# Performance work log

Measured on AMD Instinct MI355X. Metric: run time of the kernel, lower is better.

## Reference

```python
import jax, jax.numpy as jnp
import numpy as np

H = 256          # hidden_size
K = 3            # pointer hops
LAMDA = 3.0
EPS = 1e-8       # torch cosine_similarity eps
# dropout is treated as eval-mode (identity)


def _gru_cell(x, h, wi, wh, bi, bh):
    # torch GRUCell: gate order reset, update, new
    gx = x @ wi.T + bi            # (B, 3*4H)
    gh = h @ wh.T + bh
    xr, xz, xn = jnp.split(gx, 3, axis=-1)
    hr, hz, hn = jnp.split(gh, 3, axis=-1)
    r = jax.nn.sigmoid(xr + hr)
    z = jax.nn.sigmoid(xz + hz)
    n = jnp.tanh(xn + r * hn)
    return (1.0 - z) * n + z * h


def setup_inputs() -> dict:
    key = jax.random.key(0)
    ks = jax.random.split(key, 16)
    B, L = 128, 512
    d2, d4 = 2 * H, 4 * H
    sc = lambda i, shape, fan: jax.random.normal(ks[i], shape, jnp.float32) * (1.0 / np.sqrt(fan))
    return {
        "m": jax.random.normal(ks[0], (B, L, d2), jnp.float32),
        "s1": jax.random.normal(ks[1], (B, d4), jnp.float32),
        "s2": jax.random.normal(ks[2], (B, d4), jnp.float32),
        "s3": jax.random.normal(ks[3], (B, d4), jnp.float32),
        "m_mask": jnp.ones((B, L), jnp.int32),
        "w2_w": sc(4, (d2, d2), d2), "w2_b": jnp.zeros((d2,), jnp.float32),
        "w3_w": sc(5, (d4, d2), d4), "w3_b": jnp.zeros((d2,), jnp.float32),
        "w4_w": sc(6, (d4, d4), d4), "w4_b": jnp.zeros((d4,), jnp.float32),
        "w5_w": sc(7, (d4, 1), d4), "w5_b": jnp.zeros((1,), jnp.float32),
        "gru_wi": sc(8, (3 * d4, d2), d2),
        "gru_wh": sc(9, (3 * d4, d4), d4),
        "gru_bi": jnp.zeros((3 * d4,), jnp.float32),
        "gru_bh": jnp.zeros((3 * d4,), jnp.float32),
    }


def reference(m, s1, s2, s3, m_mask,
              w2_w, w2_b, w3_w, w3_b, w4_w, w4_b, w5_w, w5_b,
              gru_wi, gru_wh, gru_bi, gru_bh):
    # m: (B, L, 2H); s*: (B, 4H); m_mask: (B, L)
    mtt = m @ w2_w + w2_b                         # (B, L, 2H), loop-invariant
    m_norm = jnp.maximum(jnp.linalg.norm(mtt, axis=-1), EPS)  # (B, L)
    invalid = m_mask == 0

    def branch(st):
        for _ in range(K):
            stt = st @ w3_w + w3_b                # (B, 2H)
            s_norm = jnp.maximum(jnp.linalg.norm(stt, axis=-1), EPS)  # (B,)
            dot = jnp.einsum('bld,bd->bl', mtt, stt)
            att = LAMDA * dot / (m_norm * s_norm[:, None])
            att = jnp.where(invalid, -jnp.inf, att)
            p = jax.nn.softmax(att, axis=1)       # (B, L)
            f_att = jnp.einsum('bl,bld->bd', p, m)  # (B, 2H)
            st = _gru_cell(f_att, st, gru_wi, gru_wh, gru_bi, gru_bh)
        h = jax.nn.relu(st @ w4_w + w4_b)         # (B, 4H)
        return (h @ w5_w + w5_b)[:, 0]            # (B,)

    result = jnp.stack([branch(s1), branch(s2), branch(s3)], axis=1)  # (B, 3)
    return jax.nn.log_softmax(result, axis=1)
```

## Files before the change

kernel.cpp:

```cpp
#include <hip/hip_runtime.h>
#include <math.h>

constexpr int B  = 128;
constexpr int L  = 512;
constexpr int D2 = 512;
constexpr int D4 = 1024;
constexpr int G3 = 3072;
constexpr int R3 = 384;
constexpr int NC = 4096;
constexpr float LAMDA = 3.0f;
constexpr float EPSF  = 1e-8f;

typedef __attribute__((ext_vector_type(8))) short bf16x8;
typedef __attribute__((ext_vector_type(8))) short short8;
typedef __attribute__((ext_vector_type(4))) float f32x4;

__device__ __forceinline__ ushort f2bf(float v) {
  uint u = __builtin_bit_cast(uint, v);
  u = (u + 0x7fffu + ((u >> 16) & 1u)) >> 16;
  return (ushort)u;
}
__device__ __forceinline__ float bf2f(ushort h) {
  return __builtin_bit_cast(float, (uint)h << 16);
}
__device__ __forceinline__ float bflo(uint w) { return __builtin_bit_cast(float, w << 16); }
__device__ __forceinline__ float bfhi(uint w) { return __builtin_bit_cast(float, w & 0xffff0000u); }
__device__ __forceinline__ void split2(float v, ushort& h, ushort& l) {
  h = f2bf(v);
  l = f2bf(v - bf2f(h));
}
__device__ __forceinline__ void gload_lds16(const void* g, void* l) {
  __builtin_amdgcn_global_load_lds(
      (const __attribute__((address_space(1))) unsigned int*)g,
      (__attribute__((address_space(3))) unsigned int*)l, 16, 0, 0);
}

__global__ void k_init(const float* __restrict__ s1, const float* __restrict__ s2,
                       const float* __restrict__ s3, float* __restrict__ st3,
                       ushort* __restrict__ sth, ushort* __restrict__ stl,
                       float* __restrict__ snacc, float* __restrict__ cacc,
                       float* __restrict__ o3) {
  int idx = blockIdx.x * blockDim.x + threadIdx.x;
  if (idx < R3) { snacc[idx] = 0.f; cacc[idx] = 0.f; o3[idx] = 0.f; }
  int total = R3 * D4;
  for (; idx < total; idx += gridDim.x * blockDim.x) {
    int r = idx / D4, i = idx - r * D4;
    int k = r / B, b = r - k * B;
    const float* s = (k == 0) ? s1 : (k == 1) ? s2 : s3;
    float v = s[b * D4 + i];
    st3[idx] = v;
    if (sth) { ushort h, l; split2(v, h, l); sth[idx] = h; stl[idx] = l; }
  }
}

__global__ void k_conv_m(const float* __restrict__ m, ushort* __restrict__ mbf) {
  int idx = blockIdx.x * blockDim.x + threadIdx.x;
  const int total8 = (B * L * D2) / 8;
  for (; idx < total8; idx += gridDim.x * blockDim.x) {
    const float4* p = reinterpret_cast<const float4*>(m) + (size_t)idx * 2;
    float4 a = p[0], c = p[1];
    ushort o[8] = {f2bf(a.x), f2bf(a.y), f2bf(a.z), f2bf(a.w),
                   f2bf(c.x), f2bf(c.y), f2bf(c.z), f2bf(c.w)};
    *reinterpret_cast<uint4*>(mbf + (size_t)idx * 8) = *reinterpret_cast<const uint4*>(o);
  }
}

__global__ void k_w2t(const float* __restrict__ w2, ushort* __restrict__ w2t) {
  __shared__ ushort t[64][65];
  int bk = (blockIdx.x & 7) * 64, bn = (blockIdx.x >> 3) * 64;
  int tid = threadIdx.x;
#pragma unroll
  for (int i = 0; i < 16; ++i) {
    int e = tid + i * 256; int r = e >> 6, c = e & 63;
    t[r][c] = f2bf(w2[(bk + r) * 512 + bn + c]);
  }
  __syncthreads();
#pragma unroll
  for (int i = 0; i < 16; ++i) {
    int e = tid + i * 256; int r = e >> 6, c = e & 63;
    w2t[(bn + r) * 512 + bk + c] = t[c][r];
  }
}

__global__ void k_split_direct(const float* __restrict__ in, ushort* __restrict__ oh,
                               ushort* __restrict__ ol, int n4) {
  int idx = blockIdx.x * blockDim.x + threadIdx.x;
  for (; idx < n4; idx += gridDim.x * blockDim.x) {
    float4 v = reinterpret_cast<const float4*>(in)[idx];
    ushort4 h, l;
    split2(v.x, h.x, l.x); split2(v.y, h.y, l.y);
    split2(v.z, h.z, l.z); split2(v.w, h.w, l.w);
    reinterpret_cast<ushort4*>(oh)[idx] = h;
    reinterpret_cast<ushort4*>(ol)[idx] = l;
  }
}

__global__ void k_split_trans(const float* __restrict__ in, int K, int N,
                              ushort* __restrict__ oh, ushort* __restrict__ ol) {
  __shared__ float t[64][65];
  int bk = blockIdx.x * 64, bn = blockIdx.y * 64;
  int tid = threadIdx.x;
#pragma unroll
  for (int i = 0; i < 16; ++i) {
    int e = tid + i * 256; int r = e >> 6, c = e & 63;
    t[r][c] = in[(size_t)(bk + r) * N + bn + c];
  }
  __syncthreads();
#pragma unroll
  for (int i = 0; i < 16; ++i) {
    int e = tid + i * 256; int r = e >> 6, c = e & 63;
    ushort h, l;
    split2(t[c][r], h, l);
    oh[(size_t)(bn + r) * K + bk + c] = h;
    ol[(size_t)(bn + r) * K + bk + c] = l;
  }
}

__global__ void k_bcat2(const float* __restrict__ w3b, const float* __restrict__ gbh,
                        const float* __restrict__ w2w, float* __restrict__ bcat) {
  int idx = blockIdx.x * 256 + threadIdx.x;
  if (idx < D2) bcat[idx] = w3b[idx];
  else if (idx < D2 + G3) bcat[idx] = gbh[idx - D2];
  else if (idx < NC) {
    int e = idx - (D2 + G3);
    float s = 0.f;
    for (int d = 0; d < D2; ++d) s = fmaf(w3b[d], w2w[(size_t)e * D2 + d], s);
    bcat[idx] = s;
  }
}

__global__ __launch_bounds__(64) void k_gemm_wf(
    const ushort* __restrict__ Ahp, const ushort* __restrict__ Alp,
    const ushort* __restrict__ Bhp, const ushort* __restrict__ Blp,
    ushort* __restrict__ Ch, ushort* __restrict__ Cl) {
  const int ln = threadIdx.x;
  const int lrow = ln & 15, lk = ln >> 4;
  const int rowb = blockIdx.y * 64;
  const int colb = blockIdx.x * 64;
  size_t aoff[4], boff[4];
#pragma unroll
  for (int f = 0; f < 4; ++f) {
    aoff[f] = (size_t)(rowb + f * 16 + lrow) * D2 + lk * 8;
    boff[f] = (size_t)(colb + f * 16 + lrow) * D2 + lk * 8;
  }
  f32x4 acc[4][4] = {};
  for (int kc = 0; kc < D2; kc += 32) {
    bf16x8 ah[4], al[4], bh[4], bl[4];
#pragma unroll
    for (int f = 0; f < 4; ++f) {
      ah[f] = *reinterpret_cast<const bf16x8*>(Ahp + aoff[f] + kc);
      al[f] = *reinterpret_cast<const bf16x8*>(Alp + aoff[f] + kc);
      bh[f] = *reinterpret_cast<const bf16x8*>(Bhp + boff[f] + kc);
      bl[f] = *reinterpret_cast<const bf16x8*>(Blp + boff[f] + kc);
    }
#pragma unroll
    for (int rf = 0; rf < 4; ++rf)
#pragma unroll
      for (int cf = 0; cf < 4; ++cf) {
        acc[rf][cf] = __builtin_amdgcn_mfma_f32_16x16x32_bf16(ah[rf], bh[cf], acc[rf][cf], 0, 0, 0);
        acc[rf][cf] = __builtin_amdgcn_mfma_f32_16x16x32_bf16(al[rf], bh[cf], acc[rf][cf], 0, 0, 0);
        acc[rf][cf] = __builtin_amdgcn_mfma_f32_16x16x32_bf16(ah[rf], bl[cf], acc[rf][cf], 0, 0, 0);
      }
  }
#pragma unroll
  for (int rf = 0; rf < 4; ++rf)
#pragma unroll
    for (int cf = 0; cf < 4; ++cf) {
      int col = colb + cf * 16 + lrow;
#pragma unroll
      for (int j = 0; j < 4; ++j) {
        int row = rowb + rf * 16 + lk * 4 + j;
        ushort h, l;
        split2(acc[rf][cf][j], h, l);
        Ch[(size_t)row * D4 + col] = h;
        Cl[(size_t)row * D4 + col] = l;
      }
    }
}

__global__ __launch_bounds__(256, 2) void k_mnorm4(const ushort* __restrict__ mbf,
                                                   const ushort* __restrict__ w2t,
                                                   const float* __restrict__ b2,
                                                   float* __restrict__ norm2) {
  __shared__ ushort As[2][64 * 32];
  __shared__ ushort Bs[2][512 * 32];
  const int tid = threadIdx.x;
  const int wv = tid >> 6, ln = tid & 63;
  const int lrow = ln & 15, lk = ln >> 4;
  const size_t rowb = (size_t)blockIdx.x * 64;

  auto stage = [&](int buf, int kc) {
    {
      int li = wv * 64 + ln;
      int row = li >> 2, slot = li & 3;
      const ushort* src = mbf + (rowb + row) * 512 + kc + ((slot ^ (row & 3)) << 3);
      gload_lds16(src, &As[buf][(size_t)wv * 64 * 8]);
    }
#pragma unroll
    for (int i = 0; i < 8; ++i) {
      int c = wv * 8 + i;
      int li = c * 64 + ln;
      int col = li >> 2, slot = li & 3;
      const ushort* src = w2t + (size_t)col * 512 + kc + ((slot ^ (col & 3)) << 3);
      gload_lds16(src, &Bs[buf][(size_t)c * 64 * 8]);
    }
  };

  f32x4 acc[4][8] = {};
  stage(0, 0);
  __syncthreads();
  for (int t = 0; t < 16; ++t) {
    int cur = t & 1;
    if (t + 1 < 16) stage(cur ^ 1, (t + 1) * 32);
    bf16x8 af[4], bfr[8];
#pragma unroll
    for (int rf = 0; rf < 4; ++rf) {
      int row = rf * 16 + lrow;
      af[rf] = *reinterpret_cast<const bf16x8*>(&As[cur][row * 32 + ((lk ^ (row & 3)) << 3)]);
    }
#pragma unroll
    for (int cf = 0; cf < 8; ++cf) {
      int col = wv * 128 + cf * 16 + lrow;
      bfr[cf] = *reinterpret_cast<const bf16x8*>(&Bs[cur][col * 32 + ((lk ^ (col & 3)) << 3)]);
    }
#pragma unroll
    for (int rf = 0; rf < 4; ++rf)
#pragma unroll
      for (int cf = 0; cf < 8; ++cf)
        acc[rf][cf] = __builtin_amdgcn_mfma_f32_16x16x32_bf16(af[rf], bfr[cf], acc[rf][cf], 0, 0, 0);
    __syncthreads();
  }

  float nrm[4][4] = {};
#pragma unroll
  for (int cf = 0; cf < 8; ++cf) {
    float bb = b2[wv * 128 + cf * 16 + lrow];
#pragma unroll
    for (int rf = 0; rf < 4; ++rf)
#pragma unroll
      for (int j = 0; j < 4; ++j) {
        float v = acc[rf][cf][j] + bb;
        nrm[rf][j] = fmaf(v, v, nrm[rf][j]);
      }
  }
  __shared__ float red[4][64];
#pragma unroll
  for (int rf = 0; rf < 4; ++rf)
#pragma unroll
    for (int j = 0; j < 4; ++j) {
      float v = nrm[rf][j];
      v += __shfl_xor(v, 1); v += __shfl_xor(v, 2);
      v += __shfl_xor(v, 4); v += __shfl_xor(v, 8);
      if (lrow == 0) red[wv][rf * 16 + lk * 4 + j] = v;
    }
  __syncthreads();
  if (tid < 64)
    norm2[rowb + tid] = red[0][tid] + red[1][tid] + red[2][tid] + red[3][tid];
}

template <int EPI>
__global__ __launch_bounds__(256) void k_gemm4(
    const ushort* __restrict__ Ahp, const ushort* __restrict__ Alp,
    const ushort* __restrict__ Bhp, const ushort* __restrict__ Blp,
    int Kd, const float* __restrict__ bias,
    float* __restrict__ outf, int ldc,
    float* __restrict__ gh, float* __restrict__ shat,
    float* __restrict__ snacc, float* __restrict__ cacc,
    const float* __restrict__ b2,
    const float* __restrict__ w5w, float* __restrict__ o3) {
  __shared__ ushort AhS[2][64 * 32];
  __shared__ ushort AlS[2][64 * 32];
  __shared__ ushort BhS[2][256 * 32];
  __shared__ ushort BlS[2][256 * 32];
  const int tid = threadIdx.x;
  const int wv = tid >> 6, ln = tid & 63;
  const int lrow = ln & 15, lk = ln >> 4;
  const int rowb = blockIdx.y * 64;
  const int colb = blockIdx.x * 256;

  auto stage = [&](int buf, int kc) {
    {
      int li = wv * 64 + ln;
      int row = li >> 2, slot = li & 3;
      int s = (slot ^ (row & 3)) << 3;
      gload_lds16(Ahp + (size_t)(rowb + row) * Kd + kc + s, &AhS[buf][(size_t)wv * 64 * 8]);
      gload_lds16(Alp + (size_t)(rowb + row) * Kd + kc + s, &AlS[buf][(size_t)wv * 64 * 8]);
    }
#pragma unroll
    for (int i = 0; i < 4; ++i) {
      int c = wv * 4 + i;
      int li = c * 64 + ln;
      int col = li >> 2, slot = li & 3;
      int s = (slot ^ (col & 3)) << 3;
      gload_lds16(Bhp + (size_t)(colb + col) * Kd + kc + s, &BhS[buf][(size_t)c * 64 * 8]);
      gload_lds16(Blp + (size_t)(colb + col) * Kd + kc + s, &BlS[buf][(size_t)c * 64 * 8]);
    }
  };

  f32x4 acc[4][4] = {};
  const int nk = Kd >> 5;
  stage(0, 0);
  __syncthreads();
  for (int t = 0; t < nk; ++t) {
    int cur = t & 1;
    if (t + 1 < nk) stage(cur ^ 1, (t + 1) * 32);
    bf16x8 ah[4], al[4], bh[4], bl[4];
#pragma unroll
    for (int rf = 0; rf < 4; ++rf) {
      int row = rf * 16 + lrow;
      int off = row * 32 + ((lk ^ (row & 3)) << 3);
      ah[rf] = *reinterpret_cast<const bf16x8*>(&AhS[cur][off]);
      al[rf] = *reinterpret_cast<const bf16x8*>(&AlS[cur][off]);
    }
#pragma unroll
    for (int cf = 0; cf < 4; ++cf) {
      int col = wv * 64 + cf * 16 + lrow;
      int off = col * 32 + ((lk ^ (col & 3)) << 3);
      bh[cf] = *reinterpret_cast<const bf16x8*>(&BhS[cur][off]);
      bl[cf] = *reinterpret_cast<const bf16x8*>(&BlS[cur][off]);
    }
#pragma unroll
    for (int rf = 0; rf < 4; ++rf)
#pragma unroll
      for (int cf = 0; cf < 4; ++cf) {
        acc[rf][cf] = __builtin_amdgcn_mfma_f32_16x16x32_bf16(ah[rf], bh[cf], acc[rf][cf], 0, 0, 0);
        acc[rf][cf] = __builtin_amdgcn_mfma_f32_16x16x32_bf16(al[rf], bh[cf], acc[rf][cf], 0, 0, 0);
        acc[rf][cf] = __builtin_amdgcn_mfma_f32_16x16x32_bf16(ah[rf], bl[cf], acc[rf][cf], 0, 0, 0);
      }
    __syncthreads();
  }

  if (EPI == 0) {
#pragma unroll
    for (int rf = 0; rf < 4; ++rf)
#pragma unroll
      for (int cf = 0; cf < 4; ++cf) {
        int col = colb + wv * 64 + cf * 16 + lrow;
        float bb = bias ? bias[col] : 0.f;
#pragma unroll
        for (int j = 0; j < 4; ++j) {
          int row = rowb + rf * 16 + lk * 4 + j;
          outf[(size_t)row * ldc + col] = acc[rf][cf][j] + bb;
        }
      }
  } else if (EPI == 1) {
    if (colb < D2) {
      float ss[4][4] = {}, sc[4][4] = {};
#pragma unroll
      for (int cf = 0; cf < 4; ++cf) {
        int col = colb + wv * 64 + cf * 16 + lrow;
        float bb = bias[col], bc = b2[col];
#pragma unroll
        for (int rf = 0; rf < 4; ++rf)
#pragma unroll
          for (int j = 0; j < 4; ++j) {
            float v = acc[rf][cf][j] + bb;
            ss[rf][j] = fmaf(v, v, ss[rf][j]);
            sc[rf][j] = fmaf(v, bc, sc[rf][j]);
          }
      }
#pragma unroll
      for (int rf = 0; rf < 4; ++rf)
#pragma unroll
        for (int j = 0; j < 4; ++j) {
          float a = ss[rf][j], c = sc[rf][j];
          a += __shfl_xor(a, 1); c += __shfl_xor(c, 1);
          a += __shfl_xor(a, 2); c += __shfl_xor(c, 2);
          a += __shfl_xor(a, 4); c += __shfl_xor(c, 4);
          a += __shfl_xor(a, 8); c += __shfl_xor(c, 8);
          if (lrow == 0) {
            int row = rowb + rf * 16 + lk * 4 + j;
            atomicAdd(&snacc[row], a);
            atomicAdd(&cacc[row], c);
          }
        }
    } else {
#pragma unroll
      for (int rf = 0; rf < 4; ++rf)
#pragma unroll
        for (int cf = 0; cf < 4; ++cf) {
          int col = colb + wv * 64 + cf * 16 + lrow;
          float bb = bias[col];
#pragma unroll
          for (int j = 0; j < 4; ++j) {
            int row = rowb + rf * 16 + lk * 4 + j;
            float v = acc[rf][cf][j] + bb;
            if (col < D2 + G3) gh[(size_t)row * G3 + (col - D2)] = v;
            else               shat[(size_t)row * D2 + (col - (D2 + G3))] = v;
          }
        }
    }
  } else {
#pragma unroll
    for (int rf = 0; rf < 4; ++rf)
#pragma unroll
      for (int j = 0; j < 4; ++j) {
        float p = 0.f;
#pragma unroll
        for (int cf = 0; cf < 4; ++cf) {
          int col = colb + wv * 64 + cf * 16 + lrow;
          float v = fmaxf(acc[rf][cf][j] + bias[col], 0.f);
          p = fmaf(v, w5w[col], p);
        }
        p += __shfl_xor(p, 1); p += __shfl_xor(p, 2);
        p += __shfl_xor(p, 4); p += __shfl_xor(p, 8);
        if (lrow == 0) atomicAdd(&o3[rowb + rf * 16 + lk * 4 + j], p);
      }
  }
}

__global__ __launch_bounds__(256) void k_dot_bf(const ushort* __restrict__ mbf,
                                                const float* __restrict__ shat3,
                                                const float* __restrict__ norm2,
                                                const float* __restrict__ snacc,
                                                const float* __restrict__ cacc,
                                                const int* __restrict__ mask,
                                                float* __restrict__ att3) {
  __shared__ float sh[3][512];
  int b = blockIdx.x >> 3;
  int lt = blockIdx.x & 7;
  int tid = threadIdx.x;
  for (int k = 0; k < 3; ++k)
    for (int i = tid; i < 512; i += 256) sh[k][i] = shat3[(size_t)(k * B + b) * D2 + i];
  __syncthreads();
  int j = tid & 3, lidx = tid >> 2;
  int l = lt * 64 + lidx;
  const uint4* mrow = reinterpret_cast<const uint4*>(mbf + (size_t)(b * L + l) * D2);
  float a0 = 0.f, a1 = 0.f, a2 = 0.f;
#pragma unroll 4
  for (int s = 0; s < 16; ++s) {
    int c = s * 4 + j;
    uint4 mv = mrow[c];
    const float* p0 = &sh[0][c * 8];
    const float* p1 = &sh[1][c * 8];
    const float* p2 = &sh[2][c * 8];
    uint w[4] = {mv.x, mv.y, mv.z, mv.w};
#pragma unroll
    for (int q = 0; q < 4; ++q) {
      float lo = bflo(w[q]), hi = bfhi(w[q]);
      a0 = fmaf(lo, p0[q * 2], a0); a0 = fmaf(hi, p0[q * 2 + 1], a0);
      a1 = fmaf(lo, p1[q * 2], a1); a1 = fmaf(hi, p1[q * 2 + 1], a1);
      a2 = fmaf(lo, p2[q * 2], a2); a2 = fmaf(hi, p2[q * 2 + 1], a2);
    }
  }
  a0 += __shfl_xor(a0, 1); a0 += __shfl_xor(a0, 2);
  a1 += __shfl_xor(a1, 1); a1 += __shfl_xor(a1, 2);
  a2 += __shfl_xor(a2, 1); a2 += __shfl_xor(a2, 2);
  if (j == 0) {
    float mn = fmaxf(sqrtf(norm2[b * L + l]), EPSF);
    bool inv = (mask[b * L + l] == 0);
    float ar[3] = {a0, a1, a2};
#pragma unroll
    for (int k = 0; k < 3; ++k) {
      int r = k * B + b;
      float sn = fmaxf(sqrtf(snacc[r]), EPSF);
      float att = LAMDA * (ar[k] + cacc[r]) / (mn * sn);
      att3[(size_t)r * L + l] = inv ? -INFINITY : att;
    }
  }
}

__global__ void k_softmax(float* __restrict__ att3) {
  int r = blockIdx.x;
  float* row = att3 + (size_t)r * L;
  int tid = threadIdx.x;
  float x0 = row[tid], x1 = row[tid + 256];
  float mx = fmaxf(x0, x1);
  for (int o = 32; o; o >>= 1) mx = fmaxf(mx, __shfl_xor(mx, o));
  __shared__ float rm[4], rs[4];
  int w = tid >> 6;
  if ((tid & 63) == 0) rm[w] = mx;
  __syncthreads();
  mx = fmaxf(fmaxf(rm[0], rm[1]), fmaxf(rm[2], rm[3]));
  float e0 = expf(x0 - mx), e1 = expf(x1 - mx);
  float s = e0 + e1;
  for (int o = 32; o; o >>= 1) s += __shfl_xor(s, o);
  if ((tid & 63) == 0) rs[w] = s;
  __syncthreads();
  s = rs[0] + rs[1] + rs[2] + rs[3];
  float inv = 1.0f / s;
  row[tid] = e0 * inv;
  row[tid + 256] = e1 * inv;
}

__global__ __launch_bounds__(256) void k_fatt_bf(const ushort* __restrict__ mbf,
                                                 const float* __restrict__ p3,
                                                 ushort* __restrict__ fatth,
                                                 ushort* __restrict__ fattl) {
  __shared__ float pp[3][512];
  __shared__ float red[3][256];
  int b = blockIdx.x >> 1, dt = blockIdx.x & 1;
  int tid = threadIdx.x;
  for (int k = 0; k < 3; ++k)
    for (int i = tid; i < 512; i += 256) pp[k][i] = p3[(size_t)(k * B + b) * L + i];
  __syncthreads();
  int dpair = tid & 127, half = tid >> 7;
  int d = dt * 256 + dpair * 2;
  float a[3][2] = {};
  int l0 = half * 256;
#pragma unroll 4
  for (int l = l0; l < l0 + 256; ++l) {
    uint w = *reinterpret_cast<const uint*>(&mbf[(size_t)(b * L + l) * D2 + d]);
    float f0 = bflo(w), f1 = bfhi(w);
#pragma unroll
    for (int k = 0; k < 3; ++k) {
      float p = pp[k][l];
      a[k][0] = fmaf(p, f0, a[k][0]);
      a[k][1] = fmaf(p, f1, a[k][1]);
    }
  }
  if (half == 1) {
#pragma unroll
    for (int k = 0; k < 3; ++k) { red[k][dpair * 2] = a[k][0]; red[k][dpair * 2 + 1] = a[k][1]; }
  }
  __syncthreads();
  if (half == 0) {
#pragma unroll
    for (int k = 0; k < 3; ++k) {
      float v0 = a[k][0] + red[k][dpair * 2];
      float v1 = a[k][1] + red[k][dpair * 2 + 1];
      ushort h0, l0u, h1, l1u;
      split2(v0, h0, l0u); split2(v1, h1, l1u);
      size_t o = (size_t)(k * B + b) * D2 + d;
      fatth[o] = h0;     fattl[o] = l0u;
      fatth[o + 1] = h1; fattl[o + 1] = l1u;
    }
  }
}

__global__ void k_gates(const float* __restrict__ gx, const float* __restrict__ gh,
                        float* __restrict__ st3,
                        ushort* __restrict__ sth, ushort* __restrict__ stl,
                        float* __restrict__ snacc, float* __restrict__ cacc) {
  int idx = blockIdx.x * blockDim.x + threadIdx.x;
  if (snacc && idx < R3) { snacc[idx] = 0.f; cacc[idx] = 0.f; }
  if (idx >= R3 * D4) return;
  int r = idx / D4, i = idx - r * D4;
  const float* gxr = gx + (size_t)r * G3;
  const float* ghr = gh + (size_t)r * G3;
  float xr = gxr[i], xz = gxr[D4 + i], xn = gxr[2 * D4 + i];
  float hr = ghr[i], hz = ghr[D4 + i], hn = ghr[2 * D4 + i];
  float rr = 1.f / (1.f + expf(-(xr + hr)));
  float zz = 1.f / (1.f + expf(-(xz + hz)));
  float nn = tanhf(xn + rr * hn);
  float h = st3[idx];
  float nv = (1.f - zz) * nn + zz * h;
  st3[idx] = nv;
  if (sth) { ushort hh, ll; split2(nv, hh, ll); sth[idx] = hh; stl[idx] = ll; }
}

__global__ void k_final(const float* __restrict__ o3, const float* __restrict__ w5b,
                        float* __restrict__ out) {
  int b = threadIdx.x;
  if (b >= B) return;
  float v0 = o3[0 * B + b] + w5b[0];
  float v1 = o3[1 * B + b] + w5b[0];
  float v2 = o3[2 * B + b] + w5b[0];
  float mx = fmaxf(v0, fmaxf(v1, v2));
  float s = expf(v0 - mx) + expf(v1 - mx) + expf(v2 - mx);
  float lse = mx + logf(s);
  out[b * 3 + 0] = v0 - lse;
  out[b * 3 + 1] = v1 - lse;
  out[b * 3 + 2] = v2 - lse;
}

__global__ __launch_bounds__(256) void k_mnorm(const float* __restrict__ m,
                                               const float* __restrict__ w2,
                                               const float* __restrict__ b2,
                                               float* __restrict__ norm2) {
  __shared__ float As[64][33];
  __shared__ float Ws[32][65];
  __shared__ float red[16][64];
  const int tid = threadIdx.x;
  const int ty = tid >> 4, tx = tid & 15;
  const long rowb = (long)blockIdx.x * 64;
  float rowpart[4] = {0.f, 0.f, 0.f, 0.f};
  for (int ct = 0; ct < 8; ++ct) {
    float acc[4][4] = {};
    for (int kc = 0; kc < 16; ++kc) {
#pragma unroll
      for (int i = 0; i < 8; ++i) {
        int li = tid + i * 256;
        int r = li >> 5, c = li & 31;
        As[r][c] = m[(rowb + r) * 512 + kc * 32 + c];
      }
#pragma unroll
      for (int i = 0; i < 8; ++i) {
        int li = tid + i * 256;
        int r = li >> 6, c = li & 63;
        Ws[r][c] = w2[(kc * 32 + r) * 512 + ct * 64 + c];
      }
      __syncthreads();
#pragma unroll
      for (int k = 0; k < 32; ++k) {
        float a[4], bb[4];
#pragma unroll
        for (int i = 0; i < 4; ++i) a[i] = As[ty * 4 + i][k];
#pragma unroll
        for (int jj = 0; jj < 4; ++jj) bb[jj] = Ws[k][tx * 4 + jj];
#pragma unroll
        for (int i = 0; i < 4; ++i)
#pragma unroll
          for (int jj = 0; jj < 4; ++jj) acc[i][jj] = fmaf(a[i], bb[jj], acc[i][jj]);
      }
      __syncthreads();
    }
#pragma unroll
    for (int jj = 0; jj < 4; ++jj) {
      float bj = b2[ct * 64 + tx * 4 + jj];
#pragma unroll
      for (int i = 0; i < 4; ++i) {
        float v = acc[i][jj] + bj;
        rowpart[i] = fmaf(v, v, rowpart[i]);
      }
    }
  }
#pragma unroll
  for (int i = 0; i < 4; ++i) red[tx][ty * 4 + i] = rowpart[i];
  __syncthreads();
  if (tid < 64) {
    float s = 0.f;
#pragma unroll
    for (int t = 0; t < 16; ++t) s += red[t][tid];
    norm2[rowb + tid] = s;
  }
}

template <bool BT, int ACT>
__global__ __launch_bounds__(256) void k_gemm64(const float* __restrict__ A, int lda,
                                                const float* __restrict__ Bm, int ldb,
                                                const float* __restrict__ bias,
                                                float* __restrict__ C, int ldc, int Kd) {
  __shared__ float As[64][33];
  __shared__ float Bs[32][65];
  const int tid = threadIdx.x;
  const int ty = tid >> 4, tx = tid & 15;
  const int rowb = blockIdx.y * 64;
  const int colb = blockIdx.x * 64;
  float acc[4][4] = {};
  for (int kc = 0; kc < Kd; kc += 32) {
#pragma unroll
    for (int i = 0; i < 8; ++i) {
      int li = tid + i * 256;
      int r = li >> 5, c = li & 31;
      As[r][c] = A[(long)(rowb + r) * lda + kc + c];
    }
    if (!BT) {
#pragma unroll
      for (int i = 0; i < 8; ++i) {
        int li = tid + i * 256;
        int r = li >> 6, c = li & 63;
        Bs[r][c] = Bm[(long)(kc + r) * ldb + colb + c];
      }
    } else {
#pragma unroll
      for (int i = 0; i < 8; ++i) {
        int li = tid + i * 256;
        int n = li >> 5, k = li & 31;
        Bs[k][n] = Bm[(long)(colb + n) * ldb + kc + k];
      }
    }
    __syncthreads();
#pragma unroll
    for (int k = 0; k < 32; ++k) {
      float a[4], bb[4];
#pragma unroll
      for (int i = 0; i < 4; ++i) a[i] = As[ty * 4 + i][k];
#pragma unroll
      for (int jj = 0; jj < 4; ++jj) bb[jj] = Bs[k][tx * 4 + jj];
#pragma unroll
      for (int i = 0; i < 4; ++i)
#pragma unroll
        for (int jj = 0; jj < 4; ++jj) acc[i][jj] = fmaf(a[i], bb[jj], acc[i][jj]);
    }
    __syncthreads();
  }
#pragma unroll
  for (int i = 0; i < 4; ++i) {
    int row = rowb + ty * 4 + i;
#pragma unroll
    for (int jj = 0; jj < 4; ++jj) {
      int col = colb + tx * 4 + jj;
      float v = acc[i][jj];
      if (bias) v += bias[col];
      if (ACT == 1) v = fmaxf(v, 0.f);
      C[(long)row * ldc + col] = v;
    }
  }
}

__global__ void k_snorm(const float* __restrict__ stt3, const float* __restrict__ b2,
                        float* __restrict__ sn3, float* __restrict__ c3) {
  int r = blockIdx.x;
  int tid = threadIdx.x;
  float ss = 0.f, sc = 0.f;
  for (int j = tid; j < D2; j += 256) {
    float v = stt3[(size_t)r * D2 + j];
    ss = fmaf(v, v, ss);
    sc = fmaf(v, b2[j], sc);
  }
  for (int o = 32; o; o >>= 1) {
    ss += __shfl_down(ss, o);
    sc += __shfl_down(sc, o);
  }
  __shared__ float rs[4], rc[4];
  int w = tid >> 6;
  if ((tid & 63) == 0) { rs[w] = ss; rc[w] = sc; }
  __syncthreads();
  if (tid == 0) {
    sn3[r] = fmaxf(sqrtf(rs[0] + rs[1] + rs[2] + rs[3]), EPSF);
    c3[r] = rc[0] + rc[1] + rc[2] + rc[3];
  }
}

__global__ __launch_bounds__(256) void k_dot(const float* __restrict__ m,
                                             const float* __restrict__ shat3,
                                             const float* __restrict__ norm2,
                                             const float* __restrict__ sn3,
                                             const float* __restrict__ c3,
                                             const int* __restrict__ mask,
                                             float* __restrict__ att3) {
  __shared__ float sh[3][512];
  int b = blockIdx.x >> 3;
  int lt = blockIdx.x & 7;
  int tid = threadIdx.x;
  for (int k = 0; k < 3; ++k)
    for (int i = tid; i < 512; i += 256) sh[k][i] = shat3[(size_t)(k * B + b) * D2 + i];
  __syncthreads();
  int j = tid & 3, lidx = tid >> 2;
  int l = lt * 64 + lidx;
  const float4* mrow = reinterpret_cast<const float4*>(m + (size_t)(b * L + l) * D2);
  float a0 = 0.f, a1 = 0.f, a2 = 0.f;
#pragma unroll 8
  for (int s = 0; s < 32; ++s) {
    int d4 = s * 4 + j;
    float4 mv = mrow[d4];
    const float4 v0 = *reinterpret_cast<const float4*>(&sh[0][d4 * 4]);
    const float4 v1 = *reinterpret_cast<const float4*>(&sh[1][d4 * 4]);
    const float4 v2 = *reinterpret_cast<const float4*>(&sh[2][d4 * 4]);
    a0 += mv.x * v0.x + mv.y * v0.y + mv.z * v0.z + mv.w * v0.w;
    a1 += mv.x * v1.x + mv.y * v1.y + mv.z * v1.z + mv.w * v1.w;
    a2 += mv.x * v2.x + mv.y * v2.y + mv.z * v2.z + mv.w * v2.w;
  }
  a0 += __shfl_xor(a0, 1); a0 += __shfl_xor(a0, 2);
  a1 += __shfl_xor(a1, 1); a1 += __shfl_xor(a1, 2);
  a2 += __shfl_xor(a2, 1); a2 += __shfl_xor(a2, 2);
  if (j == 0) {
    float mn = fmaxf(sqrtf(norm2[b * L + l]), EPSF);
    bool inv = (mask[b * L + l] == 0);
    float ar[3] = {a0, a1, a2};
#pragma unroll
    for (int k = 0; k < 3; ++k) {
      int r = k * B + b;
      float att = LAMDA * (ar[k] + c3[r]) / (mn * sn3[r]);
      att3[(size_t)r * L + l] = inv ? -INFINITY : att;
    }
  }
}

__global__ __launch_bounds__(256) void k_fatt(const float* __restrict__ m,
                                              const float* __restrict__ p3,
                                              float* __restrict__ fatt3) {
  __shared__ float pp[3][512];
  __shared__ float red[3][128];
  int b = blockIdx.x >> 2, dt = blockIdx.x & 3;
  int tid = threadIdx.x;
  for (int k = 0; k < 3; ++k)
    for (int i = tid; i < 512; i += 256) pp[k][i] = p3[(size_t)(k * B + b) * L + i];
  __syncthreads();
  int d = dt * 128 + (tid & 127);
  int half = tid >> 7;
  float a0 = 0.f, a1 = 0.f, a2 = 0.f;
  int l0 = half * 256;
  for (int l = l0; l < l0 + 256; ++l) {
    float mv = m[(size_t)(b * L + l) * D2 + d];
    a0 = fmaf(pp[0][l], mv, a0);
    a1 = fmaf(pp[1][l], mv, a1);
    a2 = fmaf(pp[2][l], mv, a2);
  }
  int dd = tid & 127;
  if (half == 1) { red[0][dd] = a0; red[1][dd] = a1; red[2][dd] = a2; }
  __syncthreads();
  if (half == 0) {
    fatt3[(size_t)(0 * B + b) * D2 + d] = a0 + red[0][dd];
    fatt3[(size_t)(1 * B + b) * D2 + d] = a1 + red[1][dd];
    fatt3[(size_t)(2 * B + b) * D2 + d] = a2 + red[2][dd];
  }
}

__global__ void k_w5(const float* __restrict__ h4, const float* __restrict__ w5w,
                     float* __restrict__ o3) {
  int r = blockIdx.x, tid = threadIdx.x;
  float s = 0.f;
  for (int d = tid; d < D4; d += 256) s = fmaf(h4[(size_t)r * D4 + d], w5w[d], s);
  for (int o = 32; o; o >>= 1) s += __shfl_down(s, o);
  __shared__ float rs[4];
  if ((tid & 63) == 0) rs[tid >> 6] = s;
  __syncthreads();
  if (tid == 0) o3[r] = rs[0] + rs[1] + rs[2] + rs[3];
}

extern "C" void kernel_launch(void* const* d_in, const int* in_sizes, int n_in,
                              void* d_out, int out_size, void* d_ws, size_t ws_size,
                              hipStream_t stream) {
  const float* m    = (const float*)d_in[0];
  const float* s1   = (const float*)d_in[1];
  const float* s2   = (const float*)d_in[2];
  const float* s3   = (const float*)d_in[3];
  const int*   mask = (const int*)d_in[4];
  const float* w2w  = (const float*)d_in[5];
  const float* w2b  = (const float*)d_in[6];
  const float* w3w  = (const float*)d_in[7];
  const float* w3b  = (const float*)d_in[8];
  const float* w4w  = (const float*)d_in[9];
  const float* w4b  = (const float*)d_in[10];
  const float* w5w  = (const float*)d_in[11];
  const float* w5b  = (const float*)d_in[12];
  const float* gwi  = (const float*)d_in[13];
  const float* gwh  = (const float*)d_in[14];
  const float* gbi  = (const float*)d_in[15];
  const float* gbh  = (const float*)d_in[16];
  float* out = (float*)d_out;

  float* ws = (float*)d_ws;
  size_t off = 0;
  auto alloc = [&](size_t n) {
    float* p = ws + off;
    off += (n + 63) & ~(size_t)63;
    return p;
  };
  ushort* mbf   = (ushort*)alloc((size_t)B * L * D2 / 2);
  ushort* w2t   = (ushort*)alloc((size_t)D2 * D2 / 2);
  ushort* catBh = (ushort*)alloc((size_t)NC * D4 / 2);
  ushort* catBl = (ushort*)alloc((size_t)NC * D4 / 2);
  ushort* gxBh  = (ushort*)alloc((size_t)G3 * D2 / 2);
  ushort* gxBl  = (ushort*)alloc((size_t)G3 * D2 / 2);
  ushort* w4Bh  = (ushort*)alloc((size_t)D4 * D4 / 2);
  ushort* w4Bl  = (ushort*)alloc((size_t)D4 * D4 / 2);
  float* bcat   = alloc(NC);
  float* norm2  = alloc((size_t)B * L);
  float* st3    = alloc((size_t)R3 * D4);
  ushort* sth   = (ushort*)alloc((size_t)R3 * D4 / 2);
  ushort* stl   = (ushort*)alloc((size_t)R3 * D4 / 2);
  float* shat3  = alloc((size_t)R3 * D2);
  float* snacc  = alloc(R3);
  float* cacc   = alloc(R3);
  float* o3     = alloc(R3);
  ushort* fatth = (ushort*)alloc((size_t)R3 * D2 / 2);
  ushort* fattl = (ushort*)alloc((size_t)R3 * D2 / 2);
  float* att3   = alloc((size_t)R3 * L);
  float* gx     = alloc((size_t)R3 * G3);
  float* gh     = alloc((size_t)R3 * G3);
  const size_t big_need = off;
  const bool big = ws_size >= big_need * sizeof(float);

  if (big) {
    ushort* w2dh = (ushort*)gh;
    ushort* w2dl = w2dh + (size_t)D2 * D2;
    ushort* w3dh = (ushort*)gx;
    ushort* w3dl = w3dh + (size_t)D4 * D2;

    k_init<<<1536, 256, 0, stream>>>(s1, s2, s3, st3, sth, stl, snacc, cacc, o3);
    k_conv_m<<<2048, 256, 0, stream>>>(m, mbf);
    k_w2t<<<64, 256, 0, stream>>>(w2w, w2t);
    k_mnorm4<<<(B * L) / 64, 256, 0, stream>>>(mbf, w2t, w2b, norm2);
    k_split_trans<<<dim3(D4 / 64, D2 / 64), 256, 0, stream>>>(w3w, D4, D2, catBh, catBl);
    k_split_direct<<<1024, 256, 0, stream>>>(gwh, catBh + (size_t)D2 * D4, catBl + (size_t)D2 * D4,
                                             (G3 * D4) / 4);
    k_split_direct<<<512, 256, 0, stream>>>(gwi, gxBh, gxBl, (G3 * D2) / 4);
    k_split_trans<<<dim3(D4 / 64, D4 / 64), 256, 0, stream>>>(w4w, D4, D4, w4Bh, w4Bl);
    k_split_direct<<<256, 256, 0, stream>>>(w2w, w2dh, w2dl, (D2 * D2) / 4);
    k_split_direct<<<256, 256, 0, stream>>>(w3w, w3dh, w3dl, (D4 * D2) / 4);
    k_bcat2<<<16, 256, 0, stream>>>(w3b, gbh, w2w, bcat);
    k_gemm_wf<<<dim3(D4 / 64, D2 / 64), 64, 0, stream>>>(
        w2dh, w2dl, w3dh, w3dl,
        catBh + (size_t)(D2 + G3) * D4, catBl + (size_t)(D2 + G3) * D4);

    for (int hop = 0; hop < 3; ++hop) {
      k_gemm4<1><<<dim3(NC / 256, R3 / 64), 256, 0, stream>>>(
          sth, stl, catBh, catBl, D4, bcat, nullptr, 0,
          gh, shat3, snacc, cacc, w2b, nullptr, nullptr);
      k_dot_bf<<<B * 8, 256, 0, stream>>>(mbf, shat3, norm2, snacc, cacc, mask, att3);
      k_softmax<<<3 * B, 256, 0, stream>>>(att3);
      k_fatt_bf<<<B * 2, 256, 0, stream>>>(mbf, att3, fatth, fattl);
      k_gemm4<0><<<dim3(G3 / 256, R3 / 64), 256, 0, stream>>>(
          fatth, fattl, gxBh, gxBl, D2, gbi, gx, G3,
          nullptr, nullptr, nullptr, nullptr, nullptr, nullptr, nullptr);
      k_gates<<<1536, 256, 0, stream>>>(gx, gh, st3, sth, stl, snacc, cacc);
    }
    k_gemm4<2><<<dim3(D4 / 256, R3 / 64), 256, 0, stream>>>(
        sth, stl, w4Bh, w4Bl, D4, w4b, nullptr, 0,
        nullptr, nullptr, nullptr, nullptr, nullptr, w5w, o3);
    k_final<<<1, 128, 0, stream>>>(o3, w5b, out);
  } else {
    off = 0;
    float* f_st3   = alloc((size_t)R3 * D4);
    float* f_norm2 = alloc((size_t)B * L);
    float* f_stt   = alloc((size_t)R3 * D2);
    float* f_shat  = alloc((size_t)R3 * D2);
    float* f_sn    = alloc(R3);
    float* f_c     = alloc(R3);
    float* f_att   = alloc((size_t)R3 * L);
    float* f_fatt  = alloc((size_t)R3 * D2);
    float* f_gx    = alloc((size_t)R3 * G3);
    float* f_gh    = alloc((size_t)R3 * G3);
    float* f_h4    = alloc((size_t)R3 * D4);
    float* f_o3    = alloc(R3);
    k_init<<<1536, 256, 0, stream>>>(s1, s2, s3, f_st3, nullptr, nullptr, f_sn, f_c, f_o3);
    k_mnorm<<<(B * L) / 64, 256, 0, stream>>>(m, w2w, w2b, f_norm2);
    for (int hop = 0; hop < 3; ++hop) {
      k_gemm64<false, 0><<<dim3(D2 / 64, R3 / 64), 256, 0, stream>>>(f_st3, D4, w3w, D2, w3b, f_stt, D2, D4);
      k_snorm<<<R3, 256, 0, stream>>>(f_stt, w2b, f_sn, f_c);
      k_gemm64<true, 0><<<dim3(D2 / 64, R3 / 64), 256, 0, stream>>>(f_stt, D2, w2w, D2, nullptr, f_shat, D2, D2);
      k_dot<<<B * 8, 256, 0, stream>>>(m, f_shat, f_norm2, f_sn, f_c, mask, f_att);
      k_softmax<<<3 * B, 256, 0, stream>>>(f_att);
      k_fatt<<<B * 4, 256, 0, stream>>>(m, f_att, f_fatt);
      k_gemm64<true, 0><<<dim3(G3 / 64, R3 / 64), 256, 0, stream>>>(f_fatt, D2, gwi, D2, gbi, f_gx, G3, D2);
      k_gemm64<true, 0><<<dim3(G3 / 64, R3 / 64), 256, 0, stream>>>(f_st3, D4, gwh, D4, gbh, f_gh, G3, D4);
      k_gates<<<1536, 256, 0, stream>>>(f_gx, f_gh, f_st3, nullptr, nullptr, nullptr, nullptr);
    }
    k_gemm64<false, 1><<<dim3(D4 / 64, R3 / 64), 256, 0, stream>>>(f_st3, D4, w4w, D4, w4b, f_h4, D4, D4);
    k_w5<<<R3, 256, 0, stream>>>(f_h4, w5w, f_o3);
    k_final<<<1, 128, 0, stream>>>(f_o3, w5b, out);
  }
}
```

Baseline: 538.8 us.

## Fuse softmax into f_att kernel and use LDS-free narrower-tile split-bf16 GEMM

Replaces the LDS double-buffered 64x256 split-bf16 GEMM with a 64x128-tile variant that loads MFMA operands straight from global memory into registers, with no shared memory or barriers. Each wave now covers 32 columns, so the grids have twice as many blocks. Separately, the softmax is folded into the f_att kernel: it computes row max and exp in shared memory and scales by the inverse sum at the end, which removes one launch and one round trip of att3 per hop. The GEMM change trades explicit staging and reuse for cache-dependent direct loads, which may raise global traffic.

After: 613.3 us. 1.14x slower.

```diff
diff --git a/kernel.cpp b/kernel.cpp
--- a/kernel.cpp
+++ b/kernel.cpp
@@ -259,7 +259,7 @@
 }
 
 template <int EPI>
-__global__ __launch_bounds__(256) void k_gemm4(
+__global__ __launch_bounds__(256) void k_gemm6(
     const ushort* __restrict__ Ahp, const ushort* __restrict__ Alp,
     const ushort* __restrict__ Bhp, const ushort* __restrict__ Blp,
     int Kd, const float* __restrict__ bias,
@@ -268,74 +268,44 @@
     float* __restrict__ snacc, float* __restrict__ cacc,
     const float* __restrict__ b2,
     const float* __restrict__ w5w, float* __restrict__ o3) {
-  __shared__ ushort AhS[2][64 * 32];
-  __shared__ ushort AlS[2][64 * 32];
-  __shared__ ushort BhS[2][256 * 32];
-  __shared__ ushort BlS[2][256 * 32];
   const int tid = threadIdx.x;
   const int wv = tid >> 6, ln = tid & 63;
   const int lrow = ln & 15, lk = ln >> 4;
   const int rowb = blockIdx.y * 64;
-  const int colb = blockIdx.x * 256;
-
-  auto stage = [&](int buf, int kc) {
-    {
-      int li = wv * 64 + ln;
-      int row = li >> 2, slot = li & 3;
-      int s = (slot ^ (row & 3)) << 3;
-      gload_lds16(Ahp + (size_t)(rowb + row) * Kd + kc + s, &AhS[buf][(size_t)wv * 64 * 8]);
-      gload_lds16(Alp + (size_t)(rowb + row) * Kd + kc + s, &AlS[buf][(size_t)wv * 64 * 8]);
-    }
-#pragma unroll
-    for (int i = 0; i < 4; ++i) {
-      int c = wv * 4 + i;
-      int li = c * 64 + ln;
-      int col = li >> 2, slot = li & 3;
-      int s = (slot ^ (col & 3)) << 3;
-      gload_lds16(Bhp + (size_t)(colb + col) * Kd + kc + s, &BhS[buf][(size_t)c * 64 * 8]);
-      gload_lds16(Blp + (size_t)(colb + col) * Kd + kc + s, &BlS[buf][(size_t)c * 64 * 8]);
-    }
-  };
-
-  f32x4 acc[4][4] = {};
-  const int nk = Kd >> 5;
-  stage(0, 0);
-  __syncthreads();
-  for (int t = 0; t < nk; ++t) {
-    int cur = t & 1;
-    if (t + 1 < nk) stage(cur ^ 1, (t + 1) * 32);
-    bf16x8 ah[4], al[4], bh[4], bl[4];
-#pragma unroll
-    for (int rf = 0; rf < 4; ++rf) {
-      int row = rf * 16 + lrow;
-      int off = row * 32 + ((lk ^ (row & 3)) << 3);
-      ah[rf] = *reinterpret_cast<const bf16x8*>(&AhS[cur][off]);
-      al[rf] = *reinterpret_cast<const bf16x8*>(&AlS[cur][off]);
-    }
-#pragma unroll
-    for (int cf = 0; cf < 4; ++cf) {
-      int col = wv * 64 + cf * 16 + lrow;
-      int off = col * 32 + ((lk ^ (col & 3)) << 3);
-      bh[cf] = *reinterpret_cast<const bf16x8*>(&BhS[cur][off]);
-      bl[cf] = *reinterpret_cast<const bf16x8*>(&BlS[cur][off]);
+  const int colb = blockIdx.x * 128 + wv * 32;
+  const ushort* ah0 = Ahp + (size_t)(rowb + lrow) * Kd + lk * 8;
+  const ushort* al0 = Alp + (size_t)(rowb + lrow) * Kd + lk * 8;
+  const ushort* bh0 = Bhp + (size_t)(colb + lrow) * Kd + lk * 8;
+  const ushort* bl0 = Blp + (size_t)(colb + lrow) * Kd + lk * 8;
+  f32x4 acc[4][2] = {};
+  for (int kc = 0; kc < Kd; kc += 32) {
+    bf16x8 ah[4], al[4], bh[2], bl[2];
+#pragma unroll
+    for (int f = 0; f < 4; ++f) {
+      ah[f] = *reinterpret_cast<const bf16x8*>(ah0 + (size_t)f * 16 * Kd + kc);
+      al[f] = *reinterpret_cast<const bf16x8*>(al0 + (size_t)f * 16 * Kd + kc);
+    }
+#pragma unroll
+    for (int f = 0; f < 2; ++f) {
+      bh[f] = *reinterpret_cast<const bf16x8*>(bh0 + (size_t)f * 16 * Kd + kc);
+      bl[f] = *reinterpret_cast<const bf16x8*>(bl0 + (size_t)f * 16 * Kd + kc);
     }
 #pragma unroll
     for (int rf = 0; rf < 4; ++rf)
 #pragma unroll
-      for (int cf = 0; cf < 4; ++cf) {
+      for (int cf = 0; cf < 2; ++cf) {
         acc[rf][cf] = __builtin_amdgcn_mfma_f32_16x16x32_bf16(ah[rf], bh[cf], acc[rf][cf], 0, 0, 0);
         acc[rf][cf] = __builtin_amdgcn_mfma_f32_16x16x32_bf16(al[rf], bh[cf], acc[rf][cf], 0, 0, 0);
         acc[rf][cf] = __builtin_amdgcn_mfma_f32_16x16x32_bf16(ah[rf], bl[cf], acc[rf][cf], 0, 0, 0);
       }
-    __syncthreads();
   }
 
   if (EPI == 0) {
 #pragma unroll
     for (int rf = 0; rf < 4; ++rf)
 #pragma unroll
-      for (int cf = 0; cf < 4; ++cf) {
-        int col = colb + wv * 64 + cf * 16 + lrow;
+      for (int cf = 0; cf < 2; ++cf) {
+        int col = colb + cf * 16 + lrow;
         float bb = bias ? bias[col] : 0.f;
 #pragma unroll
         for (int j = 0; j < 4; ++j) {
@@ -347,8 +317,8 @@
     if (colb < D2) {
       float ss[4][4] = {}, sc[4][4] = {};
 #pragma unroll
-      for (int cf = 0; cf < 4; ++cf) {
-        int col = colb + wv * 64 + cf * 16 + lrow;
+      for (int cf = 0; cf < 2; ++cf) {
+        int col = colb + cf * 16 + lrow;
         float bb = bias[col], bc = b2[col];
 #pragma unroll
         for (int rf = 0; rf < 4; ++rf)
@@ -378,8 +348,8 @@
 #pragma unroll
       for (int rf = 0; rf < 4; ++rf)
 #pragma unroll
-        for (int cf = 0; cf < 4; ++cf) {
-          int col = colb + wv * 64 + cf * 16 + lrow;
+        for (int cf = 0; cf < 2; ++cf) {
+          int col = colb + cf * 16 + lrow;
           float bb = bias[col];
 #pragma unroll
           for (int j = 0; j < 4; ++j) {
@@ -397,8 +367,8 @@
       for (int j = 0; j < 4; ++j) {
         float p = 0.f;
 #pragma unroll
-        for (int cf = 0; cf < 4; ++cf) {
-          int col = colb + wv * 64 + cf * 16 + lrow;
+        for (int cf = 0; cf < 2; ++cf) {
+          int col = colb + cf * 16 + lrow;
           float v = fmaxf(acc[rf][cf][j] + bias[col], 0.f);
           p = fmaf(v, w5w[col], p);
         }
@@ -460,39 +430,35 @@
   }
 }
 
-__global__ void k_softmax(float* __restrict__ att3) {
-  int r = blockIdx.x;
-  float* row = att3 + (size_t)r * L;
-  int tid = threadIdx.x;
-  float x0 = row[tid], x1 = row[tid + 256];
-  float mx = fmaxf(x0, x1);
-  for (int o = 32; o; o >>= 1) mx = fmaxf(mx, __shfl_xor(mx, o));
-  __shared__ float rm[4], rs[4];
-  int w = tid >> 6;
-  if ((tid & 63) == 0) rm[w] = mx;
-  __syncthreads();
-  mx = fmaxf(fmaxf(rm[0], rm[1]), fmaxf(rm[2], rm[3]));
-  float e0 = expf(x0 - mx), e1 = expf(x1 - mx);
-  float s = e0 + e1;
-  for (int o = 32; o; o >>= 1) s += __shfl_xor(s, o);
-  if ((tid & 63) == 0) rs[w] = s;
-  __syncthreads();
-  s = rs[0] + rs[1] + rs[2] + rs[3];
-  float inv = 1.0f / s;
-  row[tid] = e0 * inv;
-  row[tid + 256] = e1 * inv;
-}
-
-__global__ __launch_bounds__(256) void k_fatt_bf(const ushort* __restrict__ mbf,
-                                                 const float* __restrict__ p3,
+__global__ __launch_bounds__(256) void k_fatt_sm(const ushort* __restrict__ mbf,
+                                                 const float* __restrict__ att3,
                                                  ushort* __restrict__ fatth,
                                                  ushort* __restrict__ fattl) {
   __shared__ float pp[3][512];
   __shared__ float red[3][256];
+  __shared__ float inv3[3];
   int b = blockIdx.x >> 1, dt = blockIdx.x & 1;
   int tid = threadIdx.x;
   for (int k = 0; k < 3; ++k)
-    for (int i = tid; i < 512; i += 256) pp[k][i] = p3[(size_t)(k * B + b) * L + i];
+    for (int i = tid; i < 512; i += 256) pp[k][i] = att3[(size_t)(k * B + b) * L + i];
+  __syncthreads();
+  int wv = tid >> 6, ln = tid & 63;
+  if (wv < 3) {
+    float x[8];
+#pragma unroll
+    for (int i = 0; i < 8; ++i) x[i] = pp[wv][ln + 64 * i];
+    float mx = x[0];
+#pragma unroll
+    for (int i = 1; i < 8; ++i) mx = fmaxf(mx, x[i]);
+    for (int o = 32; o; o >>= 1) mx = fmaxf(mx, __shfl_xor(mx, o));
+    float e[8], s = 0.f;
+#pragma unroll
+    for (int i = 0; i < 8; ++i) { e[i] = expf(x[i] - mx); s += e[i]; }
+    for (int o = 32; o; o >>= 1) s += __shfl_xor(s, o);
+#pragma unroll
+    for (int i = 0; i < 8; ++i) pp[wv][ln + 64 * i] = e[i];
+    if (ln == 0) inv3[wv] = 1.0f / s;
+  }
   __syncthreads();
   int dpair = tid & 127, half = tid >> 7;
   int d = dt * 256 + dpair * 2;
@@ -517,8 +483,9 @@
   if (half == 0) {
 #pragma unroll
     for (int k = 0; k < 3; ++k) {
-      float v0 = a[k][0] + red[k][dpair * 2];
-      float v1 = a[k][1] + red[k][dpair * 2 + 1];
+      float sc = inv3[k];
+      float v0 = (a[k][0] + red[k][dpair * 2]) * sc;
+      float v1 = (a[k][1] + red[k][dpair * 2 + 1]) * sc;
       ushort h0, l0u, h1, l1u;
       split2(v0, h0, l0u); split2(v1, h1, l1u);
       size_t o = (size_t)(k * B + b) * D2 + d;
@@ -756,6 +723,29 @@
       att3[(size_t)r * L + l] = inv ? -INFINITY : att;
     }
   }
+}
+
+__global__ void k_softmax(float* __restrict__ att3) {
+  int r = blockIdx.x;
+  float* row = att3 + (size_t)r * L;
+  int tid = threadIdx.x;
+  float x0 = row[tid], x1 = row[tid + 256];
+  float mx = fmaxf(x0, x1);
+  for (int o = 32; o; o >>= 1) mx = fmaxf(mx, __shfl_xor(mx, o));
+  __shared__ float rm[4], rs[4];
+  int w = tid >> 6;
+  if ((tid & 63) == 0) rm[w] = mx;
+  __syncthreads();
+  mx = fmaxf(fmaxf(rm[0], rm[1]), fmaxf(rm[2], rm[3]));
+  float e0 = expf(x0 - mx), e1 = expf(x1 - mx);
+  float s = e0 + e1;
+  for (int o = 32; o; o >>= 1) s += __shfl_xor(s, o);
+  if ((tid & 63) == 0) rs[w] = s;
+  __syncthreads();
+  s = rs[0] + rs[1] + rs[2] + rs[3];
+  float inv = 1.0f / s;
+  row[tid] = e0 * inv;
+  row[tid + 256] = e1 * inv;
 }
 
 __global__ __launch_bounds__(256) void k_fatt(const float* __restrict__ m,
@@ -877,18 +867,17 @@
         catBh + (size_t)(D2 + G3) * D4, catBl + (size_t)(D2 + G3) * D4);
 
     for (int hop = 0; hop < 3; ++hop) {
-      k_gemm4<1><<<dim3(NC / 256, R3 / 64), 256, 0, stream>>>(
+      k_gemm6<1><<<dim3(NC / 128, R3 / 64), 256, 0, stream>>>(
           sth, stl, catBh, catBl, D4, bcat, nullptr, 0,
           gh, shat3, snacc, cacc, w2b, nullptr, nullptr);
       k_dot_bf<<<B * 8, 256, 0, stream>>>(mbf, shat3, norm2, snacc, cacc, mask, att3);
-      k_softmax<<<3 * B, 256, 0, stream>>>(att3);
-      k_fatt_bf<<<B * 2, 256, 0, stream>>>(mbf, att3, fatth, fattl);
-      k_gemm4<0><<<dim3(G3 / 256, R3 / 64), 256, 0, stream>>>(
+      k_fatt_sm<<<B * 2, 256, 0, stream>>>(mbf, att3, fatth, fattl);
+      k_gemm6<0><<<dim3(G3 / 128, R3 / 64), 256, 0, stream>>>(
           fatth, fattl, gxBh, gxBl, D2, gbi, gx, G3,
           nullptr, nullptr, nullptr, nullptr, nullptr, nullptr, nullptr);
       k_gates<<<1536, 256, 0, stream>>>(gx, gh, st3, sth, stl, snacc, cacc);
     }
-    k_gemm4<2><<<dim3(D4 / 256, R3 / 64), 256, 0, stream>>>(
+    k_gemm6<2><<<dim3(D4 / 128, R3 / 64), 256, 0, stream>>>(
         sth, stl, w4Bh, w4Bl, D4, w4b, nullptr, 0,
         nullptr, nullptr, nullptr, nullptr, nullptr, w5w, o3);
     k_final<<<1, 128, 0, stream>>>(o3, w5b, out);
```
